# Kernel tuning notes

Measured on AMD Instinct MI355X. Metric: run time of the kernel, lower is better.

Reference implementation:

```python
import jax, jax.numpy as jnp
import numpy as np
from jax import lax

# Config (matches init_kwargs): TrajGRU per HKO-7 reference impl (Shi et al.)
B, T, Cin, H, W = 8, 12, 1, 128, 128
F_, L = 64, 5            # out_channels (hidden filters), num trajectories
h_, w_ = H // 2, W // 2  # post-downsample spatial size


def _conv(x, w, b, stride=1, pad=0):
    y = lax.conv_general_dilated(x, w, (stride, stride), [(pad, pad), (pad, pad)],
                                 dimension_numbers=('NCHW', 'OIHW', 'NCHW'))
    return y + b[None, :, None, None]


def _leaky(x):
    return jnp.where(x >= 0, x, 0.2 * x)  # LeakyReLU(0.2)


def _warp_multi(img, flows):
    # img: (B,C,h,w); flows: (B,L,2,h,w) pixel displacements.
    # Bilinear grid_sample with zero padding; the HKO normalization
    # (2*v/(W-1)-1) followed by align_corners=True denormalization is the
    # identity, so we sample directly at grid + flow in pixel space.
    Bb, C, Hh, Ww = img.shape
    x = jnp.arange(Ww, dtype=img.dtype)[None, None, None, :] + flows[:, :, 0]  # (B,L,h,w)
    y = jnp.arange(Hh, dtype=img.dtype)[None, None, :, None] + flows[:, :, 1]
    x0 = jnp.floor(x); y0 = jnp.floor(y)
    x1 = x0 + 1.0;     y1 = y0 + 1.0
    imgl = img.transpose(0, 2, 3, 1)  # (B,h,w,C)
    bidx = jnp.arange(Bb)[:, None, None, None]

    def gather(xi, yi):
        valid = (xi >= 0) & (xi <= Ww - 1) & (yi >= 0) & (yi <= Hh - 1)
        xic = jnp.clip(xi, 0, Ww - 1).astype(jnp.int32)
        yic = jnp.clip(yi, 0, Hh - 1).astype(jnp.int32)
        return imgl[bidx, yic, xic] * valid[..., None].astype(img.dtype)  # (B,L,h,w,C)

    wa = ((x1 - x) * (y1 - y))[..., None]
    wb = ((x1 - x) * (y - y0))[..., None]
    wc = ((x - x0) * (y1 - y))[..., None]
    wd = ((x - x0) * (y - y0))[..., None]
    out = wa * gather(x0, y0) + wb * gather(x0, y1) + wc * gather(x1, y0) + wd * gather(x1, y1)
    # concat L warped copies along channels: (B,L,h,w,C) -> (B, L*C, h, w)
    return out.transpose(0, 1, 4, 2, 3).reshape(Bb, L * C, Hh, Ww)


def setup_inputs() -> dict:
    key = jax.random.key(0)
    ks = jax.random.split(key, 13)
    def rn(k, shape, s=0.05):
        return jax.random.normal(k, shape, dtype=jnp.float32) * s
    return {
        'x': jax.random.normal(ks[0], (B, T, Cin, H, W), dtype=jnp.float32),
        'W_down': rn(ks[1], (F_ * T, Cin * T, 4, 4)),
        'b_down': rn(ks[2], (F_ * T,)),
        'W_i2h': rn(ks[3], (3 * F_, F_, 3, 3)),
        'b_i2h': rn(ks[4], (3 * F_,)),
        'W_i2f': rn(ks[5], (32, F_, 5, 5)),
        'b_i2f': rn(ks[6], (32,)),
        'W_h2f': rn(ks[7], (32, F_, 5, 5)),
        'b_h2f': rn(ks[8], (32,)),
        'W_flow': rn(ks[9], (2 * L, 32, 5, 5), 0.02),
        'b_flow': rn(ks[10], (2 * L,), 0.02),
        'W_ret': rn(ks[11], (3 * F_, L * F_, 1, 1)),
        'b_ret': rn(ks[12], (3 * F_,)),
    }


def reference(x, W_down, b_down, W_i2h, b_i2h, W_i2f, b_i2f, W_h2f, b_h2f,
              W_flow, b_flow, W_ret, b_ret):
    Bb = x.shape[0]
    # downsample conv (k=4,s=2,p=1) + LeakyReLU(0.2) on time-stacked channels
    xd = _leaky(_conv(x.reshape(Bb, T * Cin, H, W), W_down, b_down, stride=2, pad=1))
    seq = xd.reshape(Bb, T, F_, h_, w_).transpose(1, 0, 2, 3, 4)  # (T,B,F,h,w)

    # input-dependent convs are batched across all timesteps up front
    flat = seq.reshape(T * Bb, F_, h_, w_)
    i2h_all = _conv(flat, W_i2h, b_i2h, pad=1).reshape(T, Bb, 3 * F_, h_, w_)
    i2f_all = _conv(flat, W_i2f, b_i2f, pad=2).reshape(T, Bb, 32, h_, w_)

    def step(hprev, inp):
        i2h_t, i2f_t = inp
        # flow generator: leaky(i2f(x_t) + h2f(h)) -> flows conv -> L 2-ch flows
        f1 = _leaky(i2f_t + _conv(hprev, W_h2f, b_h2f, pad=2))
        flows = _conv(f1, W_flow, b_flow, pad=2).reshape(Bb, L, 2, h_, w_)
        warped = _warp_multi(hprev, -flows)          # (B, L*F, h, w)
        h2h = _conv(warped, W_ret, b_ret)            # 1x1 projection -> (B, 3F, h, w)
        ir, iu, im = jnp.split(i2h_t, 3, axis=1)
        hr, hu, hm = jnp.split(h2h, 3, axis=1)
        r = jax.nn.sigmoid(ir + hr)
        u = jax.nn.sigmoid(iu + hu)
        m = _leaky(im + r * hm)
        hnew = u * hprev + (1.0 - u) * m
        return hnew, hnew

    h0 = jnp.zeros((Bb, F_, h_, w_), x.dtype)
    _, outs = lax.scan(step, h0, (i2h_all, i2f_all))  # (T,B,F,h,w)
    return outs.transpose(1, 0, 2, 3, 4)              # (B,T,F,h,w)
```

## Files before the change

### kernel.cpp

```cpp
#include <hip/hip_runtime.h>
#include <cstdint>

typedef long long ll;
typedef __bf16 bf16x8 __attribute__((ext_vector_type(8)));
typedef float f32x4 __attribute__((ext_vector_type(4)));
typedef unsigned int u32x4 __attribute__((ext_vector_type(4)));

#define NB 8
#define NT 12
#define NF 64
#define HWSZ 4096
#define I2H_T ((ll)NB * 4096 * 192)
#define I2F_T ((ll)NB * 4096 * 32)

struct alignas(8)  bh4 { __bf16 h[4]; };
struct alignas(16) bh8 { __bf16 h[8]; };

static __device__ inline f32x4 mfma16(bf16x8 a, bf16x8 b, f32x4 c) {
  return __builtin_amdgcn_mfma_f32_16x16x32_bf16(a, b, c, 0, 0, 0);
}
static __device__ inline bf16x8 ld8(const __bf16* p) {
  u32x4 u = *(const u32x4*)p;
  return __builtin_bit_cast(bf16x8, u);
}
static __device__ inline void st4(__bf16* p, float a0, float a1, float a2, float a3) {
  bh4 t; t.h[0] = (__bf16)a0; t.h[1] = (__bf16)a1; t.h[2] = (__bf16)a2; t.h[3] = (__bf16)a3;
  *(bh4*)p = t;
}
static __device__ inline float lky(float a) { return a >= 0.f ? a : 0.2f * a; }

static __device__ inline int swz_bid() {
  int bid = blockIdx.x;
  return ((gridDim.x & 7) == 0) ? (bid & 7) * (gridDim.x >> 3) + (bid >> 3) : bid;
}

static __device__ inline void step_decode(int& b, int& y, int& xh) {
  int bid = blockIdx.x;
  int oct = bid & 7, s = bid >> 3;
  b = s >> 4;
  int r = s & 15;
  y = oct * 8 + (r >> 1);
  xh = r & 1;
}

template<int W, int HALO>
static __device__ void stage8(__bf16* dst, const __bf16* grow) {
  int tid = threadIdx.x;
  u32x4 zz = {0u, 0u, 0u, 0u};
  #pragma unroll
  for (int it = 0; it < 2; ++it) {
    int i = tid + it * 256;
    int xr = i >> 3, g = i & 7, xi = xr + HALO;
    u32x4 v = zz;
    if (grow) v = *(const u32x4*)(grow + xr * 64 + g * 8);
    *(u32x4*)(dst + (g * W + xi) * 8) = v;
  }
  if (tid < 16 * HALO) {
    int h = tid >> 3, g = tid & 7;
    int xi = (h < HALO) ? h : 64 + h;
    *(u32x4*)(dst + (g * W + xi) * 8) = zz;
  }
}

__global__ __launch_bounds__(256) void k_prep(
    const float* __restrict__ Wd, const float* __restrict__ Wc,
    const float* __restrict__ Wi, const float* __restrict__ Wh,
    const float* __restrict__ Wfl, const float* __restrict__ Wret,
    __bf16* __restrict__ Adown, __bf16* __restrict__ Ai2h,
    __bf16* __restrict__ Afi, __bf16* __restrict__ Afh,
    __bf16* __restrict__ Afl, __bf16* __restrict__ Aret) {
  int n = blockIdx.x * 256 + threadIdx.x;
  if (n < 147456) {
    Adown[n] = (__bf16)Wd[n];
  } else if (n < 258048) {
    int i = n - 147456;
    int tap = i / 12288, o = (i % 12288) / 64, c = i % 64;
    Ai2h[i] = (__bf16)Wc[(o * 64 + c) * 9 + tap];
  } else if (n < 309248) {
    int i = n - 258048;
    int tap = i / 2048, o = (i % 2048) / 64, c = i % 64;
    Afi[i] = (__bf16)Wi[(o * 64 + c) * 25 + tap];
  } else if (n < 360448) {
    int i = n - 309248;
    int tap = i / 2048, o = (i % 2048) / 64, c = i % 64;
    Afh[i] = (__bf16)Wh[(o * 64 + c) * 25 + tap];
  } else if (n < 373248) {
    int i = n - 360448;
    int tap = i / 512, o = (i % 512) / 32, c = i % 32;
    Afl[i] = (__bf16)(o < 10 ? Wfl[(o * 32 + c) * 25 + tap] : 0.f);
  } else if (n < 434688) {
    Aret[n - 373248] = (__bf16)Wret[n - 373248];
  }
}

__global__ __launch_bounds__(256) void k_down(
    const float* __restrict__ x, const __bf16* __restrict__ Adown,
    const float* __restrict__ bd, __bf16* __restrict__ seq) {
  __shared__ __bf16 smd[6240];
  int bi = swz_bid();
  int zQ = bi & 3, y = (bi >> 2) & 63, b = bi >> 8;
  int tid = threadIdx.x;
  for (int i = tid; i < 6240; i += 256) {
    int ic = i / 520, rem = i % 520, ky = rem / 130, xi = rem % 130;
    int ix = xi - 1, iy = 2 * y - 1 + ky;
    float v = (ix >= 0 && ix < 128 && iy >= 0 && iy < 128)
                  ? x[(((ll)(b * 12 + ic) * 128 + iy) << 7) + ix] : 0.f;
    smd[i] = (__bf16)v;
  }
  __syncthreads();
  int wv = __builtin_amdgcn_readfirstlane(tid >> 6);
  int lane = tid & 63, q = lane >> 4, lr = lane & 15;
  int px = wv * 16 + lr;
  f32x4 zv = {0.f, 0.f, 0.f, 0.f};
  f32x4 acc[12];
  #pragma unroll
  for (int mt = 0; mt < 12; ++mt) acc[mt] = zv;

  for (int ks = 0; ks < 6; ++ks) {
    int k0 = ks * 32 + q * 8;
    int ic = k0 >> 4, ky0 = (k0 >> 2) & 3;
    const __bf16* rp = smd + (ic * 4 + ky0) * 130 + 2 * px;
    bh8 bb;
    #pragma unroll
    for (int j = 0; j < 8; ++j)
      bb.h[j] = rp[(j >> 2) * 130 + (j & 3)];
    bf16x8 bfr = __builtin_bit_cast(bf16x8, bb);
    #pragma unroll
    for (int mt = 0; mt < 12; ++mt) {
      bf16x8 afr = ld8(Adown + ((ll)(zQ * 192 + mt * 16 + lr) * 192 + k0));
      acc[mt] = mfma16(afr, bfr, acc[mt]);
    }
  }
  #pragma unroll
  for (int mt = 0; mt < 12; ++mt) {
    int t_idx = zQ * 3 + (mt >> 2);
    int f0 = (mt & 3) * 16 + q * 4;
    float v[4];
    #pragma unroll
    for (int r = 0; r < 4; ++r)
      v[r] = lky(acc[mt][r] + bd[zQ * 192 + mt * 16 + q * 4 + r]);
    st4(seq + (((ll)(t_idx * NB + b) * 4096 + y * 64 + px) * 64 + f0),
        v[0], v[1], v[2], v[3]);
  }
}

__global__ __launch_bounds__(256, 2) void k_i2h4(
    const __bf16* __restrict__ in0, const __bf16* __restrict__ A,
    const float* __restrict__ bc, __bf16* __restrict__ out0) {
  __shared__ __align__(16) __bf16 smI[6 * 8 * 67 * 8];
  __shared__ __align__(16) __bf16 smA[2][96 * 64];
  int bi_ = swz_bid();
  int yg = bi_ & 15, och = (bi_ >> 4) & 1, tb = bi_ >> 5;
  int y0 = yg * 4;
  const __bf16* base = in0 + (ll)tb * (4096 * 64);
  const __bf16* Ab = A + ((ll)och * 96) * 64;
  int tid = threadIdx.x;
  u32x4 ar[3];
  auto loadA = [&](int tap) {
    #pragma unroll
    for (int it = 0; it < 3; ++it) {
      int j = it * 256 + tid;
      ar[it] = *(const u32x4*)(Ab + (ll)tap * (192 * 64) + j * 8);
    }
  };
  auto writeA = [&](int buf) {
    #pragma unroll
    for (int it = 0; it < 3; ++it) {
      int j = it * 256 + tid;
      int oc = j >> 3, g = j & 7;
      *(u32x4*)(smA[buf] + oc * 64 + ((g ^ (oc & 7)) * 8)) = ar[it];
    }
  };
  loadA(0);
  #pragma unroll
  for (int s = 0; s < 6; ++s) {
    int yr = y0 - 1 + s;
    stage8<67, 1>(smI + s * (8 * 67 * 8),
                  (yr >= 0 && yr < 64) ? base + (ll)yr * 64 * 64 : nullptr);
  }
  writeA(0);
  __syncthreads();

  int wv = __builtin_amdgcn_readfirstlane(tid >> 6);
  int lane = tid & 63, q = lane >> 4, lr = lane & 15;
  int mh = wv & 1, rg = wv >> 1;
  f32x4 zv = {0.f, 0.f, 0.f, 0.f};
  f32x4 acc[3][8];
  #pragma unroll
  for (int mt = 0; mt < 3; ++mt)
    #pragma unroll
    for (int nt = 0; nt < 8; ++nt) acc[mt][nt] = zv;

  for (int tap = 0; tap < 9; ++tap) {
    if (tap < 8) loadA(tap + 1);
    int ky = tap / 3, kx = tap % 3;
    const __bf16* Ax = smA[tap & 1];
    __builtin_amdgcn_s_setprio(1);
    #pragma unroll
    for (int ks = 0; ks < 2; ++ks) {
      bf16x8 afr[3];
      #pragma unroll
      for (int mt = 0; mt < 3; ++mt) {
        int oc = mh * 48 + mt * 16 + lr;
        afr[mt] = ld8(Ax + oc * 64 + (((ks * 4 + q) ^ (lr & 7)) * 8));
      }
      bf16x8 bfr[8];
      #pragma unroll
      for (int rl = 0; rl < 2; ++rl)
        #pragma unroll
        for (int nx = 0; nx < 4; ++nx) {
          int s = rg * 2 + rl + ky;
          bfr[rl * 4 + nx] =
              ld8(smI + ((s * 8 + ks * 4 + q) * 67 + nx * 16 + lr + kx) * 8);
        }
      #pragma unroll
      for (int mt = 0; mt < 3; ++mt)
        #pragma unroll
        for (int nt = 0; nt < 8; ++nt)
          acc[mt][nt] = mfma16(afr[mt], bfr[nt], acc[mt][nt]);
    }
    __builtin_amdgcn_s_setprio(0);
    if (tap < 8) writeA((tap + 1) & 1);
    __syncthreads();
  }

  #pragma unroll
  for (int rl = 0; rl < 2; ++rl)
    #pragma unroll
    for (int nx = 0; nx < 4; ++nx) {
      int row = y0 + rg * 2 + rl, px = nx * 16 + lr;
      __bf16* op = out0 + ((ll)tb * 4096 + row * 64 + px) * 192;
      #pragma unroll
      for (int mt = 0; mt < 3; ++mt) {
        int oc0 = och * 96 + mh * 48 + mt * 16 + q * 4;
        f32x4 a = acc[mt][rl * 4 + nx];
        st4(op + oc0, a[0] + bc[oc0], a[1] + bc[oc0 + 1],
                      a[2] + bc[oc0 + 2], a[3] + bc[oc0 + 3]);
      }
    }
}

__global__ __launch_bounds__(256, 2) void k_i2fb(
    const __bf16* __restrict__ in0, const __bf16* __restrict__ A,
    __bf16* __restrict__ out0) {
  __shared__ __align__(16) __bf16 smI[8 * 8 * 69 * 8];
  __shared__ __align__(16) __bf16 smA[2][32 * 64];
  float* red = (float*)smI;
  int bi_ = swz_bid();
  int yg = bi_ & 15, tb = bi_ >> 4;
  int y0 = yg * 4;
  const __bf16* base = in0 + (ll)tb * (4096 * 64);
  int tid = threadIdx.x;
  u32x4 ar;
  auto loadA = [&](int tap) { ar = *(const u32x4*)(A + (ll)tap * 2048 + tid * 8); };
  auto writeA = [&](int buf) {
    int oc = tid >> 3, g = tid & 7;
    *(u32x4*)(smA[buf] + oc * 64 + ((g ^ (oc & 7)) * 8)) = ar;
  };
  loadA(0);
  #pragma unroll
  for (int s = 0; s < 8; ++s) {
    int yr = y0 - 2 + s;
    stage8<69, 2>(smI + s * (8 * 69 * 8),
                  (yr >= 0 && yr < 64) ? base + (ll)yr * 64 * 64 : nullptr);
  }
  writeA(0);
  __syncthreads();

  int wv = __builtin_amdgcn_readfirstlane(tid >> 6);
  int lane = tid & 63, q = lane >> 4, lr = lane & 15;
  int rg = wv & 1, ksh = wv >> 1;
  f32x4 zv = {0.f, 0.f, 0.f, 0.f};
  f32x4 acc[2][8];
  #pragma unroll
  for (int mt = 0; mt < 2; ++mt)
    #pragma unroll
    for (int nt = 0; nt < 8; ++nt) acc[mt][nt] = zv;

  for (int tap = 0; tap < 25; ++tap) {
    if (tap < 24) loadA(tap + 1);
    int ky = tap / 5, kx = tap % 5;
    const __bf16* Ax = smA[tap & 1];
    __builtin_amdgcn_s_setprio(1);
    bf16x8 afr[2];
    #pragma unroll
    for (int mt = 0; mt < 2; ++mt) {
      int oc = mt * 16 + lr;
      afr[mt] = ld8(Ax + oc * 64 + (((ksh * 4 + q) ^ (lr & 7)) * 8));
    }
    bf16x8 bfr[8];
    #pragma unroll
    for (int rl = 0; rl < 2; ++rl)
      #pragma unroll
      for (int nx = 0; nx < 4; ++nx) {
        int s = rg * 2 + rl + ky;
        bfr[rl * 4 + nx] =
            ld8(smI + ((s * 8 + ksh * 4 + q) * 69 + nx * 16 + lr + kx) * 8);
      }
    #pragma unroll
    for (int mt = 0; mt < 2; ++mt)
      #pragma unroll
      for (int nt = 0; nt < 8; ++nt)
        acc[mt][nt] = mfma16(afr[mt], bfr[nt], acc[mt][nt]);
    __builtin_amdgcn_s_setprio(0);
    if (tap < 24) writeA((tap + 1) & 1);
    __syncthreads();
  }

  if (ksh == 1) {
    #pragma unroll
    for (int mt = 0; mt < 2; ++mt)
      #pragma unroll
      for (int rl = 0; rl < 2; ++rl)
        #pragma unroll
        for (int nx = 0; nx < 4; ++nx) {
          int row_l = rg * 2 + rl, px = nx * 16 + lr;
          int oc = mt * 16 + q * 4;
          f32x4 a = acc[mt][rl * 4 + nx];
          #pragma unroll
          for (int r = 0; r < 4; ++r)
            red[(row_l * 64 + px) * 33 + oc + r] = a[r];
        }
  }
  __syncthreads();
  if (ksh == 0) {
    #pragma unroll
    for (int mt = 0; mt < 2; ++mt)
      #pragma unroll
      for (int rl = 0; rl < 2; ++rl)
        #pragma unroll
        for (int nx = 0; nx < 4; ++nx) {
          int row_l = rg * 2 + rl, px = nx * 16 + lr;
          int oc0 = mt * 16 + q * 4;
          f32x4 a = acc[mt][rl * 4 + nx];
          float v[4];
          #pragma unroll
          for (int r = 0; r < 4; ++r)
            v[r] = a[r] + red[(row_l * 64 + px) * 33 + oc0 + r];
          st4(out0 + ((ll)tb * 4096 + (y0 + row_l) * 64 + px) * 32 + oc0,
              v[0], v[1], v[2], v[3]);
        }
  }
}

#define STEP_SMEM_BYTES (25344 + 2176)

static __device__ void dev_h2f(char* smraw, int t0,
    const __bf16* __restrict__ hb, const __bf16* __restrict__ A,
    const float* __restrict__ bi, const float* __restrict__ bh,
    const __bf16* __restrict__ i2f_t, __bf16* __restrict__ f1buf,
    int b, int y, int xh) {
  __bf16* smI = (__bf16*)smraw;
  float* red = (float*)smraw;
  int x0 = xh * 32;
  int tid = threadIdx.x;
  int wv = __builtin_amdgcn_readfirstlane(tid >> 6);
  int lane = tid & 63, q = lane >> 4, lr = lane & 15;

  int pxl_e = tid >> 3, oc0_e = (tid & 7) * 4;
  bh4 iv = *(const bh4*)(i2f_t + ((ll)(b * 64 + y) * 64 + x0 + pxl_e) * 32 + oc0_e);

  bf16x8 cur[2][2], nxt[2][2];
  auto loadAt = [&](int tap, bf16x8 a[2][2]) {
    #pragma unroll
    for (int ks = 0; ks < 2; ++ks)
      #pragma unroll
      for (int mt = 0; mt < 2; ++mt)
        a[ks][mt] = ld8(A + ((ll)(tap * 32 + mt * 16 + lr) * 64 + ks * 32 + q * 8));
  };
  loadAt(wv, cur);

  u32x4 zz = {0u, 0u, 0u, 0u};
  for (int i = tid; i < 5 * 296; i += 256) {
    int s = i / 296, rem = i % 296, xi = rem >> 3, g = rem & 7;
    int yr = y - 2 + s, xg = x0 - 2 + xi;
    u32x4 v = zz;
    if (!t0 && yr >= 0 && yr < 64 && xg >= 0 && xg < 64)
      v = *(const u32x4*)(hb + ((ll)(b * 64 + yr) * 64 + xg) * 64 + g * 8);
    *(u32x4*)(smI + ((s * 8 + g) * 37 + xi) * 8) = v;
  }
  __syncthreads();

  f32x4 zv = {0.f, 0.f, 0.f, 0.f};
  f32x4 acc[2][2];
  #pragma unroll
  for (int mt = 0; mt < 2; ++mt)
    #pragma unroll
    for (int nx = 0; nx < 2; ++nx) acc[mt][nx] = zv;

  #pragma unroll
  for (int j = 0; j < 7; ++j) {
    int tap = 4 * j + wv;
    if (tap < 25) {
      if (tap + 4 < 25) loadAt(tap + 4, nxt);
      int ky = tap / 5, kx = tap % 5;
      #pragma unroll
      for (int ks = 0; ks < 2; ++ks) {
        bf16x8 bfr[2];
        #pragma unroll
        for (int nx = 0; nx < 2; ++nx)
          bfr[nx] = ld8(smI + ((ky * 8 + ks * 4 + q) * 37 + nx * 16 + lr + kx) * 8);
        #pragma unroll
        for (int mt = 0; mt < 2; ++mt)
          #pragma unroll
          for (int nx = 0; nx < 2; ++nx)
            acc[mt][nx] = mfma16(cur[ks][mt], bfr[nx], acc[mt][nx]);
      }
      #pragma unroll
      for (int ks = 0; ks < 2; ++ks)
        #pragma unroll
        for (int mt = 0; mt < 2; ++mt) cur[ks][mt] = nxt[ks][mt];
    }
  }
  __syncthreads();

  #pragma unroll
  for (int mt = 0; mt < 2; ++mt)
    #pragma unroll
    for (int nx = 0; nx < 2; ++nx) {
      int pxl = nx * 16 + lr, oc = mt * 16 + q * 4;
      f32x4 a = acc[mt][nx];
      #pragma unroll
      for (int r = 0; r < 4; ++r)
        red[wv * 1056 + pxl * 33 + oc + r] = a[r];
    }
  __syncthreads();

  float v[4];
  #pragma unroll
  for (int r = 0; r < 4; ++r) {
    float s = red[0 * 1056 + pxl_e * 33 + oc0_e + r] + red[1 * 1056 + pxl_e * 33 + oc0_e + r] +
              red[2 * 1056 + pxl_e * 33 + oc0_e + r] + red[3 * 1056 + pxl_e * 33 + oc0_e + r];
    v[r] = lky(s + (float)iv.h[r] + bi[oc0_e + r] + bh[oc0_e + r]);
  }
  st4(f1buf + ((ll)(b * 64 + y) * 64 + x0 + pxl_e) * 32 + oc0_e, v[0], v[1], v[2], v[3]);
}

static __device__ void dev_fwr(char* smraw, int t0,
    const __bf16* __restrict__ f1buf, const __bf16* __restrict__ Afl,
    const float* __restrict__ bfl, const __bf16* __restrict__ hb,
    const __bf16* __restrict__ Aret, const float* __restrict__ br,
    const __bf16* __restrict__ i2h_t, const float* __restrict__ hprevf,
    float* __restrict__ outp, ll osb, __bf16* __restrict__ hbc,
    int b, int y, int xh) {
  float* flows = (float*)(smraw + 25344);
  __bf16* f1l = (__bf16*)smraw;
  __bf16* wrp = (__bf16*)smraw;
  int x0 = xh * 32;
  int tid = threadIdx.x;
  int wv = __builtin_amdgcn_readfirstlane(tid >> 6);
  int lane = tid & 63, q = lane >> 4, lr = lane & 15;

  int f0w = wv * 16 + q * 4;
  bh4 irv[2], iuv[2], imv[2];
  float h04[2][4];
  #pragma unroll
  for (int nt = 0; nt < 2; ++nt) {
    int xg = x0 + nt * 16 + lr;
    const __bf16* ih = i2h_t + ((ll)(b * 64 + y) * 64 + xg) * 192;
    irv[nt] = *(const bh4*)(ih + f0w);
    iuv[nt] = *(const bh4*)(ih + 64 + f0w);
    imv[nt] = *(const bh4*)(ih + 128 + f0w);
    const float* hp = hprevf + (ll)b * osb + y * 64 + xg;
    #pragma unroll
    for (int r = 0; r < 4; ++r)
      h04[nt][r] = t0 ? 0.f : hp[(ll)(f0w + r) << 12];
  }

  u32x4 zz = {0u, 0u, 0u, 0u};
  for (int i = tid; i < 5 * 148; i += 256) {
    int s = i / 148, rem = i % 148, xi = rem >> 2, g = rem & 3;
    int yr = y - 2 + s, xg = x0 - 2 + xi;
    u32x4 v = zz;
    if (yr >= 0 && yr < 64 && xg >= 0 && xg < 64)
      v = *(const u32x4*)(f1buf + ((ll)(b * 64 + yr) * 64 + xg) * 32 + g * 8);
    *(u32x4*)(f1l + ((s * 4 + g) * 37 + xi) * 8) = v;
  }
  __syncthreads();

  if (wv < 2) {
    f32x4 acc1 = {0.f, 0.f, 0.f, 0.f};
    #pragma unroll
    for (int tap = 0; tap < 25; ++tap) {
      int ky = tap / 5, kx = tap % 5;
      bf16x8 bfr = ld8(f1l + ((ky * 4 + q) * 37 + wv * 16 + lr + kx) * 8);
      bf16x8 afr = ld8(Afl + ((ll)(tap * 16 + lr) * 32 + q * 8));
      acc1 = mfma16(afr, bfr, acc1);
    }
    #pragma unroll
    for (int r = 0; r < 4; ++r) {
      int oc = q * 4 + r;
      flows[(wv * 16 + lr) * 17 + oc] = acc1[r] + (oc < 10 ? bfl[oc] : 0.f);
    }
  }
  __syncthreads();

  bf16x8 cR[3], nR[3];
  auto loadAr = [&](int ks, bf16x8* a) {
    #pragma unroll
    for (int mt = 0; mt < 3; ++mt)
      a[mt] = ld8(Aret + ((ll)(mt * 64 + wv * 16 + lr) * 320 + ks * 32 + q * 8));
  };
  loadAr(0, cR);

  {
    int pxl = tid & 31, cg = tid >> 5;
    int xw = x0 + pxl;
    const __bf16* hbb = hb + ((ll)b << 18);
    #pragma unroll
    for (int l = 0; l < 5; ++l) {
      bh8 ov;
      if (t0) {
        #pragma unroll
        for (int i = 0; i < 8; ++i) ov.h[i] = (__bf16)0.f;
      } else {
        float fx = flows[pxl * 17 + 2 * l];
        float fy = flows[pxl * 17 + 2 * l + 1];
        float pxf = (float)xw - fx, pyf = (float)y - fy;
        float x0f = floorf(pxf), y0f = floorf(pyf);
        int xx0 = (int)x0f, yy0 = (int)y0f, xx1 = xx0 + 1, yy1 = yy0 + 1;
        float dx = pxf - x0f, dy = pyf - y0f;
        bool vx0 = xx0 >= 0 && xx0 <= 63, vx1 = xx1 >= 0 && xx1 <= 63;
        bool vy0 = yy0 >= 0 && yy0 <= 63, vy1 = yy1 >= 0 && yy1 <= 63;
        float wA = (vx0 && vy0) ? (1.f - dx) * (1.f - dy) : 0.f;
        float wB = (vx0 && vy1) ? (1.f - dx) * dy : 0.f;
        float wC = (vx1 && vy0) ? dx * (1.f - dy) : 0.f;
        float wD = (vx1 && vy1) ? dx * dy : 0.f;
        int cx0 = min(max(xx0, 0), 63), cx1 = min(max(xx1, 0), 63);
        int cy0 = min(max(yy0, 0), 63), cy1 = min(max(yy1, 0), 63);
        int o00 = (cy0 * 64 + cx0) * 64, o10 = (cy1 * 64 + cx0) * 64;
        int o01 = (cy0 * 64 + cx1) * 64, o11 = (cy1 * 64 + cx1) * 64;
        int c0 = cg * 8;
        bf16x8 aA = ld8(hbb + o00 + c0), aB = ld8(hbb + o10 + c0);
        bf16x8 aC = ld8(hbb + o01 + c0), aD = ld8(hbb + o11 + c0);
        #pragma unroll
        for (int i = 0; i < 8; ++i)
          ov.h[i] = (__bf16)(wA * (float)aA[i] + wB * (float)aB[i] +
                             wC * (float)aC[i] + wD * (float)aD[i]);
      }
      int G = l * 8 + cg;
      int Gs = (G & ~7) | ((G & 7) ^ (pxl & 7));
      *(bh8*)(wrp + (pxl * 40 + Gs) * 8) = ov;
    }
  }
  __syncthreads();

  f32x4 zv = {0.f, 0.f, 0.f, 0.f};
  f32x4 racc[3][2];
  #pragma unroll
  for (int mt = 0; mt < 3; ++mt)
    #pragma unroll
    for (int nt = 0; nt < 2; ++nt) racc[mt][nt] = zv;
  #pragma unroll
  for (int ks = 0; ks < 10; ++ks) {
    if (ks < 9) loadAr(ks + 1, nR);
    bf16x8 bfr[2];
    #pragma unroll
    for (int nt = 0; nt < 2; ++nt) {
      int pxl = nt * 16 + lr;
      int Gr = ks * 4 + q;
      int Gs = (Gr & ~7) | ((Gr & 7) ^ (pxl & 7));
      bfr[nt] = ld8(wrp + (pxl * 40 + Gs) * 8);
    }
    #pragma unroll
    for (int mt = 0; mt < 3; ++mt)
      #pragma unroll
      for (int nt = 0; nt < 2; ++nt)
        racc[mt][nt] = mfma16(cR[mt], bfr[nt], racc[mt][nt]);
    #pragma unroll
    for (int mt = 0; mt < 3; ++mt) cR[mt] = nR[mt];
  }

  #pragma unroll
  for (int nt = 0; nt < 2; ++nt) {
    int xg = x0 + nt * 16 + lr;
    float* ob = outp + (ll)b * osb + y * 64 + xg;
    float hn4[4];
    #pragma unroll
    for (int r = 0; r < 4; ++r) {
      int f = f0w + r;
      float hr = racc[0][nt][r] + br[f];
      float hu = racc[1][nt][r] + br[f + 64];
      float hm = racc[2][nt][r] + br[f + 128];
      float rr = 1.f / (1.f + __expf(-((float)irv[nt].h[r] + hr)));
      float uu = 1.f / (1.f + __expf(-((float)iuv[nt].h[r] + hu)));
      float m = lky((float)imv[nt].h[r] + rr * hm);
      float hn = uu * h04[nt][r] + (1.f - uu) * m;
      ob[(ll)f << 12] = hn;
      hn4[r] = hn;
    }
    st4(hbc + ((ll)(b * 64 + y) * 64 + xg) * 64 + f0w,
        hn4[0], hn4[1], hn4[2], hn4[3]);
  }
}

__global__ __launch_bounds__(256, 4) void k_h2f5(
    int t0, const __bf16* hb, const __bf16* A, const float* bi, const float* bh,
    const __bf16* i2f_t, __bf16* f1buf) {
  __shared__ __align__(16) char smraw[STEP_SMEM_BYTES];
  int b, y, xh;
  step_decode(b, y, xh);
  dev_h2f(smraw, t0, hb, A, bi, bh, i2f_t, f1buf, b, y, xh);
}

__global__ __launch_bounds__(256, 4) void k_fwr2(
    int t0, const __bf16* f1buf, const __bf16* Afl, const float* bfl,
    const __bf16* hb, const __bf16* Aret, const float* br,
    const __bf16* i2h_t, const float* hprevf,
    float* outp, ll osb, __bf16* hbc) {
  __shared__ __align__(16) char smraw[STEP_SMEM_BYTES];
  int b, y, xh;
  step_decode(b, y, xh);
  dev_fwr(smraw, t0, f1buf, Afl, bfl, hb, Aret, br, i2h_t, hprevf,
          outp, osb, hbc, b, y, xh);
}

extern "C" void kernel_launch(void* const* d_in, const int* in_sizes, int n_in,
                              void* d_out, int out_size, void* d_ws, size_t ws_size,
                              hipStream_t stream) {
  const float* x      = (const float*)d_in[0];
  const float* W_down = (const float*)d_in[1];
  const float* b_down = (const float*)d_in[2];
  const float* W_i2h  = (const float*)d_in[3];
  const float* b_i2h  = (const float*)d_in[4];
  const float* W_i2f  = (const float*)d_in[5];
  const float* b_i2f  = (const float*)d_in[6];
  const float* W_h2f  = (const float*)d_in[7];
  const float* b_h2f  = (const float*)d_in[8];
  const float* W_flow = (const float*)d_in[9];
  const float* b_flow = (const float*)d_in[10];
  const float* W_ret  = (const float*)d_in[11];
  const float* b_ret  = (const float*)d_in[12];
  float* out = (float*)d_out;

  const ll H_N = (ll)NB * 4096 * 64;

  auto align256 = [](ll v) { return (v + 255) & ~255LL; };
  ll fixed = 0;
  fixed += align256(147456LL * 2);
  fixed += align256(110592LL * 2);
  fixed += align256(51200LL * 2) * 2;
  fixed += align256(12800LL * 2);
  fixed += align256(61440LL * 2);
  fixed += align256((ll)NT * NB * 4096 * 64 * 2);
  fixed += align256((ll)NB * 4096 * 32 * 2);
  fixed += align256(H_N * 2) * 2;
  ll need_full = fixed + align256(NT * I2H_T * 2) + align256(NT * I2F_T * 2);
  int fits = (need_full <= (ll)ws_size);
  int slabT = fits ? NT : 1;

  char* p = (char*)d_ws;
  auto alloc = [&](ll bytes) { char* r = p; p += (bytes + 255) & ~255LL; return r; };
  __bf16* Adown  = (__bf16*)alloc(147456LL * 2);
  __bf16* Ai2h   = (__bf16*)alloc(110592LL * 2);
  __bf16* Afi    = (__bf16*)alloc(51200LL * 2);
  __bf16* Afh    = (__bf16*)alloc(51200LL * 2);
  __bf16* Afl    = (__bf16*)alloc(12800LL * 2);
  __bf16* Aret   = (__bf16*)alloc(61440LL * 2);
  __bf16* seq    = (__bf16*)alloc((ll)NT * NB * 4096 * 64 * 2);
  __bf16* f1buf  = (__bf16*)alloc((ll)NB * 4096 * 32 * 2);
  __bf16* hbufA  = (__bf16*)alloc(H_N * 2);
  __bf16* hbufB  = (__bf16*)alloc(H_N * 2);
  __bf16* i2h_sl = (__bf16*)alloc(slabT * I2H_T * 2);
  __bf16* i2f_sl = (__bf16*)alloc(slabT * I2F_T * 2);
  if (p > (char*)d_ws + ws_size) return;

  k_prep<<<1698, 256, 0, stream>>>(W_down, W_i2h, W_i2f, W_h2f, W_flow, W_ret,
                                   Adown, Ai2h, Afi, Afh, Afl, Aret);
  k_down<<<NB * 64 * 4, 256, 0, stream>>>(x, Adown, b_down, seq);

  if (fits) {
    k_i2h4<<<NT * NB * 2 * 16, 256, 0, stream>>>(seq, Ai2h, b_i2h, i2h_sl);
    k_i2fb<<<NT * NB * 16, 256, 0, stream>>>(seq, Afi, i2f_sl);
  }

  const ll osb = (ll)NT * NF * HWSZ;
  for (int t = 0; t < NT; ++t) {
    const __bf16* xt0 = seq + (ll)t * NB * 4096 * 64;
    if (!fits) {
      k_i2h4<<<NB * 2 * 16, 256, 0, stream>>>(xt0, Ai2h, b_i2h, i2h_sl);
      k_i2fb<<<NB * 16, 256, 0, stream>>>(xt0, Afi, i2f_sl);
    }
    int ti = fits ? t : 0;
    const __bf16* hb = (t & 1) ? hbufA : hbufB;
    __bf16* hbc = (t & 1) ? hbufB : hbufA;
    const float* hpf = (t == 0) ? out : out + (ll)(t - 1) * NF * HWSZ;

    k_h2f5<<<NB * 64 * 2, 256, 0, stream>>>((t == 0) ? 1 : 0, hb, Afh,
                                            b_i2f, b_h2f,
                                            i2f_sl + (ll)ti * I2F_T, f1buf);
    k_fwr2<<<NB * 64 * 2, 256, 0, stream>>>((t == 0) ? 1 : 0, f1buf, Afl,
                                            b_flow, hb, Aret, b_ret,
                                            i2h_sl + (ll)ti * I2H_T, hpf,
                                            out + (ll)t * NF * HWSZ, osb, hbc);
  }
}
```

Before: 823.6 us.

## Overlap i2h/i2f convs for step t+2 with recurrent step kernels

Only the first two timesteps of the input-to-hidden and input-to-flow convolutions are now precomputed up front. The convolutions for timestep t+2 run as extra blocks appended to the h2f and fwr step kernels, which otherwise leave compute idle. This hides the batched-conv cost inside the sequential recurrence. In exchange the step kernels get more blocks and, for k_h2f5, a larger shared-memory allocation, which can lower occupancy.

```diff
diff --git a/kernel.cpp b/kernel.cpp
--- a/kernel.cpp
+++ b/kernel.cpp
@@ -57,6 +57,23 @@
   }
   if (tid < 16 * HALO) {
     int h = tid >> 3, g = tid & 7;
+    int xi = (h < HALO) ? h : 64 + h;
+    *(u32x4*)(dst + (g * W + xi) * 8) = zz;
+  }
+}
+
+template<int W, int HALO>
+static __device__ void stage_half(__bf16* dst, const __bf16* grow, int goff) {
+  int tid = threadIdx.x;
+  u32x4 zz = {0u, 0u, 0u, 0u};
+  {
+    int xr = tid >> 2, g = tid & 3, xi = xr + HALO;
+    u32x4 v = zz;
+    if (grow) v = *(const u32x4*)(grow + xr * 64 + (goff + g) * 8);
+    *(u32x4*)(dst + (g * W + xi) * 8) = v;
+  }
+  if (tid < 8 * HALO) {
+    int h = tid >> 2, g = tid & 3;
     int xi = (h < HALO) ? h : 64 + h;
     *(u32x4*)(dst + (g * W + xi) * 8) = zz;
   }
@@ -343,6 +360,147 @@
   }
 }
 
+static __device__ void dev_i2h_lite(char* smraw,
+    const __bf16* __restrict__ xt2, const __bf16* __restrict__ A,
+    const float* __restrict__ bc, __bf16* __restrict__ out0, int cbid) {
+  __bf16* smI = (__bf16*)smraw;
+  int och = cbid & 1, yp = (cbid >> 1) & 31, b = cbid >> 6;
+  int y0 = yp * 2;
+  const __bf16* base = xt2 + (ll)b * (4096 * 64);
+  int tid = threadIdx.x;
+  int wv = __builtin_amdgcn_readfirstlane(tid >> 6);
+  int lane = tid & 63, q = lane >> 4, lr = lane & 15;
+  int mh = wv & 1, rg = wv >> 1;
+
+  bf16x8 cA[3], nA[3];
+  auto loadA = [&](int kk, bf16x8* a) {
+    int tap = kk >> 1, ks = kk & 1;
+    #pragma unroll
+    for (int mt = 0; mt < 3; ++mt)
+      a[mt] = ld8(A + ((ll)(tap * 192 + och * 96 + mh * 48 + mt * 16 + lr)) * 64 +
+                  ks * 32 + q * 8);
+  };
+  loadA(0, cA);
+  #pragma unroll
+  for (int s = 0; s < 4; ++s) {
+    int yr = y0 - 1 + s;
+    stage8<67, 1>(smI + s * (8 * 67 * 8),
+                  (yr >= 0 && yr < 64) ? base + (ll)yr * 64 * 64 : nullptr);
+  }
+  __syncthreads();
+
+  f32x4 zv = {0.f, 0.f, 0.f, 0.f};
+  f32x4 acc[3][4];
+  #pragma unroll
+  for (int mt = 0; mt < 3; ++mt)
+    #pragma unroll
+    for (int nt = 0; nt < 4; ++nt) acc[mt][nt] = zv;
+
+  #pragma unroll
+  for (int kk = 0; kk < 18; ++kk) {
+    if (kk < 17) loadA(kk + 1, nA);
+    int tap = kk >> 1, ks = kk & 1;
+    int ky = tap / 3, kx = tap % 3;
+    bf16x8 bfr[4];
+    #pragma unroll
+    for (int nt = 0; nt < 4; ++nt) {
+      int s = rg + ky;
+      bfr[nt] = ld8(smI + ((s * 8 + ks * 4 + q) * 67 + nt * 16 + lr + kx) * 8);
+    }
+    #pragma unroll
+    for (int mt = 0; mt < 3; ++mt)
+      #pragma unroll
+      for (int nt = 0; nt < 4; ++nt)
+        acc[mt][nt] = mfma16(cA[mt], bfr[nt], acc[mt][nt]);
+    #pragma unroll
+    for (int mt = 0; mt < 3; ++mt) cA[mt] = nA[mt];
+  }
+
+  int row = y0 + rg;
+  #pragma unroll
+  for (int nt = 0; nt < 4; ++nt) {
+    int px = nt * 16 + lr;
+    __bf16* op = out0 + ((ll)b * 4096 + row * 64 + px) * 192;
+    #pragma unroll
+    for (int mt = 0; mt < 3; ++mt) {
+      int oc0 = och * 96 + mh * 48 + mt * 16 + q * 4;
+      f32x4 a = acc[mt][nt];
+      st4(op + oc0, a[0] + bc[oc0], a[1] + bc[oc0 + 1],
+                    a[2] + bc[oc0 + 2], a[3] + bc[oc0 + 3]);
+    }
+  }
+}
+
+static __device__ void dev_i2f_lite(char* smraw,
+    const __bf16* __restrict__ xt2, const __bf16* __restrict__ A,
+    __bf16* __restrict__ out0, int cbid) {
+  __bf16* smI = (__bf16*)smraw;
+  int yp = cbid & 31, b = cbid >> 5;
+  int y0 = yp * 2;
+  const __bf16* base = xt2 + (ll)b * (4096 * 64);
+  int tid = threadIdx.x;
+  int wv = __builtin_amdgcn_readfirstlane(tid >> 6);
+  int lane = tid & 63, q = lane >> 4, lr = lane & 15;
+  int rg = wv & 1, xh = wv >> 1;
+
+  f32x4 zv = {0.f, 0.f, 0.f, 0.f};
+  f32x4 acc[2][2];
+  #pragma unroll
+  for (int mt = 0; mt < 2; ++mt)
+    #pragma unroll
+    for (int nt = 0; nt < 2; ++nt) acc[mt][nt] = zv;
+
+  bf16x8 cA[2], nA[2];
+  #pragma unroll
+  for (int ks = 0; ks < 2; ++ks) {
+    if (ks) __syncthreads();
+    #pragma unroll
+    for (int s = 0; s < 6; ++s) {
+      int yr = y0 - 2 + s;
+      stage_half<69, 2>(smI + s * (4 * 69 * 8),
+                        (yr >= 0 && yr < 64) ? base + (ll)yr * 64 * 64 : nullptr,
+                        ks * 4);
+    }
+    auto loadA = [&](int tap, bf16x8* a) {
+      #pragma unroll
+      for (int mt = 0; mt < 2; ++mt)
+        a[mt] = ld8(A + ((ll)(tap * 32 + mt * 16 + lr)) * 64 + ks * 32 + q * 8);
+    };
+    loadA(0, cA);
+    __syncthreads();
+    #pragma unroll
+    for (int tap = 0; tap < 25; ++tap) {
+      if (tap < 24) loadA(tap + 1, nA);
+      int ky = tap / 5, kx = tap % 5;
+      bf16x8 bfr[2];
+      #pragma unroll
+      for (int nt = 0; nt < 2; ++nt) {
+        int s = rg + ky;
+        bfr[nt] = ld8(smI + ((s * 4 + q) * 69 + xh * 32 + nt * 16 + lr + kx) * 8);
+      }
+      #pragma unroll
+      for (int mt = 0; mt < 2; ++mt)
+        #pragma unroll
+        for (int nt = 0; nt < 2; ++nt)
+          acc[mt][nt] = mfma16(cA[mt], bfr[nt], acc[mt][nt]);
+      cA[0] = nA[0]; cA[1] = nA[1];
+    }
+  }
+
+  int row = y0 + rg;
+  #pragma unroll
+  for (int nt = 0; nt < 2; ++nt) {
+    int px = xh * 32 + nt * 16 + lr;
+    __bf16* op = out0 + ((ll)b * 4096 + row * 64 + px) * 32;
+    #pragma unroll
+    for (int mt = 0; mt < 2; ++mt) {
+      int oc0 = mt * 16 + q * 4;
+      f32x4 a = acc[mt][nt];
+      st4(op + oc0, a[0], a[1], a[2], a[3]);
+    }
+  }
+}
+
 #define STEP_SMEM_BYTES (25344 + 2176)
 
 static __device__ void dev_h2f(char* smraw, int t0,
@@ -596,23 +754,33 @@
 
 __global__ __launch_bounds__(256, 4) void k_h2f5(
     int t0, const __bf16* hb, const __bf16* A, const float* bi, const float* bh,
-    const __bf16* i2f_t, __bf16* f1buf) {
-  __shared__ __align__(16) char smraw[STEP_SMEM_BYTES];
-  int b, y, xh;
-  step_decode(b, y, xh);
-  dev_h2f(smraw, t0, hb, A, bi, bh, i2f_t, f1buf, b, y, xh);
+    const __bf16* i2f_t, __bf16* f1buf,
+    const __bf16* xt2, const __bf16* Ai2h, const float* bc2, __bf16* i2h_out) {
+  __shared__ __align__(16) char smraw[34304];
+  if (blockIdx.x < 1024) {
+    int b, y, xh;
+    step_decode(b, y, xh);
+    dev_h2f(smraw, t0, hb, A, bi, bh, i2f_t, f1buf, b, y, xh);
+  } else {
+    dev_i2h_lite(smraw, xt2, Ai2h, bc2, i2h_out, blockIdx.x - 1024);
+  }
 }
 
 __global__ __launch_bounds__(256, 4) void k_fwr2(
     int t0, const __bf16* f1buf, const __bf16* Afl, const float* bfl,
     const __bf16* hb, const __bf16* Aret, const float* br,
     const __bf16* i2h_t, const float* hprevf,
-    float* outp, ll osb, __bf16* hbc) {
+    float* outp, ll osb, __bf16* hbc,
+    const __bf16* xt2, const __bf16* Afi, __bf16* i2f_out) {
   __shared__ __align__(16) char smraw[STEP_SMEM_BYTES];
-  int b, y, xh;
-  step_decode(b, y, xh);
-  dev_fwr(smraw, t0, f1buf, Afl, bfl, hb, Aret, br, i2h_t, hprevf,
-          outp, osb, hbc, b, y, xh);
+  if (blockIdx.x < 1024) {
+    int b, y, xh;
+    step_decode(b, y, xh);
+    dev_fwr(smraw, t0, f1buf, Afl, bfl, hb, Aret, br, i2h_t, hprevf,
+            outp, osb, hbc, b, y, xh);
+  } else {
+    dev_i2f_lite(smraw, xt2, Afi, i2f_out, blockIdx.x - 1024);
+  }
 }
 
 extern "C" void kernel_launch(void* const* d_in, const int* in_sizes, int n_in,
@@ -670,15 +838,15 @@
   k_down<<<NB * 64 * 4, 256, 0, stream>>>(x, Adown, b_down, seq);
 
   if (fits) {
-    k_i2h4<<<NT * NB * 2 * 16, 256, 0, stream>>>(seq, Ai2h, b_i2h, i2h_sl);
-    k_i2fb<<<NT * NB * 16, 256, 0, stream>>>(seq, Afi, i2f_sl);
+    k_i2h4<<<2 * NB * 32, 256, 0, stream>>>(seq, Ai2h, b_i2h, i2h_sl);
+    k_i2fb<<<2 * NB * 16, 256, 0, stream>>>(seq, Afi, i2f_sl);
   }
 
   const ll osb = (ll)NT * NF * HWSZ;
   for (int t = 0; t < NT; ++t) {
     const __bf16* xt0 = seq + (ll)t * NB * 4096 * 64;
     if (!fits) {
-      k_i2h4<<<NB * 2 * 16, 256, 0, stream>>>(xt0, Ai2h, b_i2h, i2h_sl);
+      k_i2h4<<<NB * 32, 256, 0, stream>>>(xt0, Ai2h, b_i2h, i2h_sl);
       k_i2fb<<<NB * 16, 256, 0, stream>>>(xt0, Afi, i2f_sl);
     }
     int ti = fits ? t : 0;
@@ -686,12 +854,20 @@
     __bf16* hbc = (t & 1) ? hbufB : hbufA;
     const float* hpf = (t == 0) ? out : out + (ll)(t - 1) * NF * HWSZ;
 
-    k_h2f5<<<NB * 64 * 2, 256, 0, stream>>>((t == 0) ? 1 : 0, hb, Afh,
-                                            b_i2f, b_h2f,
-                                            i2f_sl + (ll)ti * I2F_T, f1buf);
-    k_fwr2<<<NB * 64 * 2, 256, 0, stream>>>((t == 0) ? 1 : 0, f1buf, Afl,
-                                            b_flow, hb, Aret, b_ret,
-                                            i2h_sl + (ll)ti * I2H_T, hpf,
-                                            out + (ll)t * NF * HWSZ, osb, hbc);
-  }
-}
+    int t2 = t + 2;
+    int carry = (fits && t2 < NT) ? 1 : 0;
+    const __bf16* xt2 = carry ? seq + (ll)t2 * NB * 4096 * 64 : nullptr;
+    __bf16* i2h_o = carry ? i2h_sl + (ll)t2 * I2H_T : nullptr;
+    __bf16* i2f_o = carry ? i2f_sl + (ll)t2 * I2F_T : nullptr;
+
+    k_h2f5<<<1024 + (carry ? 512 : 0), 256, 0, stream>>>(
+        (t == 0) ? 1 : 0, hb, Afh, b_i2f, b_h2f,
+        i2f_sl + (ll)ti * I2F_T, f1buf,
+        xt2, Ai2h, b_i2h, i2h_o);
+    k_fwr2<<<1024 + (carry ? 256 : 0), 256, 0, stream>>>(
+        (t == 0) ? 1 : 0, f1buf, Afl, b_flow, hb, Aret, b_ret,
+        i2h_sl + (ll)ti * I2H_T, hpf,
+        out + (ll)t * NF * HWSZ, osb, hbc,
+        xt2, Afi, i2f_o);
+  }
+}
```

New measurement: 1.249 ms. 51.7% more time.
